# Kernel optimization log

Measured on AMD Instinct MI355X. Metric: run time of the kernel, lower is better.

## Reference

```python
import jax, jax.numpy as jnp
import numpy as np
import math

B, S, D = 4, 2048, 1024
H, DK, DV = 16, 64, 64
EPS = 1e-5
SCALE = math.sqrt(1.0 / D)  # NOTE: original scales by 1/sqrt(d_model), not 1/sqrt(d_k)


def setup_inputs() -> dict:
    key = jax.random.key(0)
    ks = jax.random.split(key, 12)
    s = 0.02
    return {
        "Q": jax.random.normal(ks[0], (B, S, D), jnp.float32),
        "K": jax.random.normal(ks[1], (B, S, D), jnp.float32),
        "V": jax.random.normal(ks[2], (B, S, D), jnp.float32),
        # stacked per-head projection weights (torch Linear: y = x @ W.T + b)
        "Wq": jax.random.normal(ks[3], (H, D, DK), jnp.float32) * s,
        "bq": jnp.zeros((H, DK), jnp.float32),
        "Wk": jax.random.normal(ks[4], (H, D, DK), jnp.float32) * s,
        "bk": jnp.zeros((H, DK), jnp.float32),
        "Wv": jax.random.normal(ks[5], (H, D, DV), jnp.float32) * s,
        "bv": jnp.zeros((H, DV), jnp.float32),
        "Wo": jax.random.normal(ks[6], (H * DV, D), jnp.float32) * s,
        "bo": jnp.zeros((D,), jnp.float32),
        "gamma": jnp.ones((D,), jnp.float32),
        "beta": jnp.zeros((D,), jnp.float32),
    }


def reference(Q, K, V, Wq, bq, Wk, bk, Wv, bv, Wo, bo, gamma, beta):
    residual = Q
    # batched per-head projections: [B,S,D] x [H,D,dk] -> [B,H,S,dk]
    q = jnp.einsum("bsd,hdk->bhsk", Q, Wq) + bq[None, :, None, :]
    k = jnp.einsum("bsd,hdk->bhsk", K, Wk) + bk[None, :, None, :]
    v = jnp.einsum("bsd,hdv->bhsv", V, Wv) + bv[None, :, None, :]
    # scaled dot-product attention (scale uses d_model, per original code)
    attn = jax.nn.softmax(jnp.einsum("bhsk,bhtk->bhst", q, k) * SCALE, axis=-1)
    out = jnp.einsum("bhst,bhtv->bhsv", attn, v)  # [B,H,S,DV]
    # concat heads along feature dim: [B,S,H*DV]
    out = out.transpose(0, 2, 1, 3).reshape(B, S, H * DV)
    out = out @ Wo + bo  # output projection
    # dropout is identity in eval mode
    out = out + residual
    # BatchNorm1d over (B,S) per channel (training-mode batch stats)
    mean = jnp.mean(out, axis=(0, 1))
    var = jnp.mean(jnp.square(out - mean), axis=(0, 1))
    out = (out - mean) * jax.lax.rsqrt(var + EPS) * gamma + beta
    return out.transpose(0, 2, 1)  # (B, d_model, S)
```

## Files before the change

### kernel.cpp

```cpp
#include <hip/hip_runtime.h>

#define B_ 4
#define S_ 2048
#define D_ 1024
#define H_ 16
#define SCALE_ 0.03125f
#define EPS_ 1e-5f
#define NBS_ 8192

typedef unsigned short ushort_t;
typedef __attribute__((ext_vector_type(8))) short short8;
typedef __attribute__((ext_vector_type(4))) short short4v;
typedef __attribute__((ext_vector_type(4))) float floatx4;
typedef __attribute__((ext_vector_type(2))) unsigned int uint2v;

__device__ __forceinline__ ushort_t f2bf(float f) {
  union { float f; unsigned u; } v; v.f = f;
  unsigned r = v.u + 0x7fffu + ((v.u >> 16) & 1u);
  return (ushort_t)(r >> 16);
}

__device__ __forceinline__ float fast_exp2(float x) {
#if __has_builtin(__builtin_amdgcn_exp2f)
  return __builtin_amdgcn_exp2f(x);
#else
  return __expf(x * 0.6931471805599453f);
#endif
}

__device__ __forceinline__ unsigned cvt_pk_bf16(float a, float b) {
  unsigned r;
  asm("v_cvt_pk_bf16_f32 %0, %1, %2" : "=v"(r) : "v"(a), "v"(b));
  return r;
}

__device__ __forceinline__ short8 cvt8(float4 a, float4 b) {
  short8 r;
  r[0] = (short)f2bf(a.x); r[1] = (short)f2bf(a.y);
  r[2] = (short)f2bf(a.z); r[3] = (short)f2bf(a.w);
  r[4] = (short)f2bf(b.x); r[5] = (short)f2bf(b.y);
  r[6] = (short)f2bf(b.z); r[7] = (short)f2bf(b.w);
  return r;
}

__device__ __forceinline__ void gload16(const void* g, void* l) {
  __builtin_amdgcn_global_load_lds(
      (const __attribute__((address_space(1))) unsigned int*)g,
      (__attribute__((address_space(3))) unsigned int*)l, 16, 0, 0);
}

__global__ __launch_bounds__(256) void cvtx_k(const float* __restrict__ src,
                                              ushort_t* __restrict__ dst)
{
  size_t i = ((size_t)blockIdx.x * 256 + threadIdx.x) * 8;
  float4 a = *(const float4*)(src + i);
  float4 b = *(const float4*)(src + i + 4);
  *(short8*)(dst + i) = cvt8(a, b);
}

__global__ __launch_bounds__(256) void wtr_k(const float* __restrict__ src,
                                             ushort_t* __restrict__ dst, int mode)
{
  __shared__ float t[64][65];
  const int tr = blockIdx.x, tc = blockIdx.y;
  const float* sb; int sld;
  if (mode == 0) { sb = src + (size_t)tr * 65536 + (size_t)tc * 64 * 64; sld = 64; }
  else           { sb = src + (size_t)tc * 64 * 1024 + (size_t)tr * 64;  sld = 1024; }
  const int tid = threadIdx.x;
  const int rr = tid >> 2, cs = (tid & 3) * 16;
  const float* p = sb + (size_t)rr * sld + cs;
#pragma unroll
  for (int j = 0; j < 16; ++j) t[rr][cs + j] = p[j];
  __syncthreads();
  ushort_t* dp = dst + (size_t)(tr * 64 + rr) * 1024 + tc * 64 + cs;
#pragma unroll
  for (int j = 0; j < 16; ++j) dp[j] = f2bf(t[cs + j][rr]);
}

__device__ __forceinline__ void xcd_tile(int id, int& m0, int& n0)
{
  m0 = ((id & 7) + 8 * (id >> 6)) * 128;
  n0 = ((id >> 3) & 7) * 128;
}

__device__ __forceinline__ void gemm_mainloop(
    const ushort_t* __restrict__ A, const ushort_t* __restrict__ Bw,
    ushort_t* As, ushort_t* Bs,
    int m0, int n0, int wv, int lane, floatx4 acc[4][2])
{
  const int quad = lane >> 4, l16 = lane & 15;
  const int wm = wv & 1, wn = wv >> 1;
  const int r8 = lane >> 3;
  const int kx = ((lane & 7) ^ r8) * 8;

  auto stage = [&](int buf, int k0) {
#pragma unroll
    for (int j = 0; j < 2; ++j) {
      const int rb = (wv * 2 + j) * 8;
      gload16(A + (size_t)(m0 + rb + r8) * 1024 + k0 + kx,
              (char*)As + buf * 16384 + rb * 128);
      gload16(Bw + (size_t)(n0 + rb + r8) * 1024 + k0 + kx,
              (char*)Bs + buf * 16384 + rb * 128);
    }
  };

  stage(0, 0);
  __syncthreads();

  const int swz = (l16 & 7) << 4;
  for (int it = 0; it < 16; ++it) {
    const int cur = it & 1;
    if (it < 15) stage(cur ^ 1, (it + 1) * 64);
    const char* Ab = (const char*)As + cur * 16384;
    const char* Bb = (const char*)Bs + cur * 16384;
#pragma unroll
    for (int hf = 0; hf < 2; ++hf) {
      short8 af[4], bf[2];
      const int C = (hf * 64 + quad * 16) ^ swz;
#pragma unroll
      for (int i = 0; i < 4; ++i)
        af[i] = *(const short8*)(Ab + (wm * 64 + i * 16 + l16) * 128 + C);
#pragma unroll
      for (int i = 0; i < 2; ++i)
        bf[i] = *(const short8*)(Bb + (wn * 32 + i * 16 + l16) * 128 + C);
#pragma unroll
      for (int mi = 0; mi < 4; ++mi)
#pragma unroll
        for (int ni = 0; ni < 2; ++ni)
          acc[mi][ni] = __builtin_amdgcn_mfma_f32_16x16x32_bf16(
              af[mi], bf[ni], acc[mi][ni], 0, 0, 0);
    }
    __syncthreads();
  }
}

__global__ __launch_bounds__(512) void gemm_proj(
    const ushort_t* __restrict__ A, const ushort_t* __restrict__ Bw,
    const float* __restrict__ bias, ushort_t* __restrict__ outp, float scale)
{
  __shared__ ushort_t As[2 * 128 * 64];
  __shared__ ushort_t Bs[2 * 128 * 64];
  const int tid = threadIdx.x;
  const int wv = tid >> 6, lane = tid & 63, quad = lane >> 4, l16 = lane & 15;
  int m0, n0;
  xcd_tile(blockIdx.x, m0, n0);
  const int wm = wv & 1, wn = wv >> 1;

  floatx4 acc[4][2];
#pragma unroll
  for (int i = 0; i < 4; ++i)
#pragma unroll
    for (int j = 0; j < 2; ++j) acc[i][j] = (floatx4){0.f, 0.f, 0.f, 0.f};

  gemm_mainloop(A, Bw, As, Bs, m0, n0, wv, lane, acc);

  const int b = m0 >> 11;
  const int sbase = (m0 & 2047) + wm * 64;
#pragma unroll
  for (int ni = 0; ni < 2; ++ni) {
    const int c = n0 + wn * 32 + ni * 16 + l16;
    const int h = c >> 6, nn = c & 63;
    const float bs = bias[c];
    ushort_t* op = outp + (size_t)(b * 16 + h) * 2048 * 64 + nn;
#pragma unroll
    for (int mi = 0; mi < 4; ++mi)
#pragma unroll
      for (int r = 0; r < 4; ++r) {
        int s = sbase + mi * 16 + quad * 4 + r;
        op[(size_t)s * 64] = f2bf((acc[mi][ni][r] + bs) * scale);
      }
  }
}

__global__ __launch_bounds__(512) void gemm_projT(
    const ushort_t* __restrict__ A, const ushort_t* __restrict__ Bw,
    const float* __restrict__ bias, ushort_t* __restrict__ outp)
{
  __shared__ ushort_t As[2 * 128 * 64];
  __shared__ ushort_t Bs[2 * 128 * 64];
  const int tid = threadIdx.x;
  const int wv = tid >> 6, lane = tid & 63, quad = lane >> 4, l16 = lane & 15;
  int m0, n0;
  xcd_tile(blockIdx.x, m0, n0);
  const int wm = wv & 1, wn = wv >> 1;

  floatx4 acc[4][2];
#pragma unroll
  for (int i = 0; i < 4; ++i)
#pragma unroll
    for (int j = 0; j < 2; ++j) acc[i][j] = (floatx4){0.f, 0.f, 0.f, 0.f};

  gemm_mainloop(A, Bw, As, Bs, m0, n0, wv, lane, acc);

  const int b = m0 >> 11;
  const int sbase = (m0 & 2047) + wm * 64;
#pragma unroll
  for (int ni = 0; ni < 2; ++ni) {
    const int c = n0 + wn * 32 + ni * 16 + l16;
    const int h = c >> 6, nn = c & 63;
    const float bs = bias[c];
    ushort_t* op = outp + ((size_t)(b * 16 + h) * 64 + nn) * 2048;
#pragma unroll
    for (int mi = 0; mi < 4; ++mi) {
      int s0v = sbase + mi * 16 + quad * 4;
      short4v p;
#pragma unroll
      for (int r = 0; r < 4; ++r) p[r] = (short)f2bf(acc[mi][ni][r] + bs);
      *(short4v*)(op + s0v) = p;
    }
  }
}

__global__ __launch_bounds__(512) void gemm_oproj(
    const ushort_t* __restrict__ A, const ushort_t* __restrict__ Bw,
    const float* __restrict__ bo, const float* __restrict__ resid,
    float* __restrict__ y, float* __restrict__ s1, float* __restrict__ s2)
{
  __shared__ ushort_t As[2 * 128 * 64];
  __shared__ ushort_t Bs[2 * 128 * 64];
  const int tid = threadIdx.x;
  const int wv = tid >> 6, lane = tid & 63, quad = lane >> 4, l16 = lane & 15;
  int m0, n0;
  xcd_tile(blockIdx.x, m0, n0);
  const int wm = wv & 1, wn = wv >> 1;

  floatx4 acc[4][2];
#pragma unroll
  for (int i = 0; i < 4; ++i)
#pragma unroll
    for (int j = 0; j < 2; ++j) acc[i][j] = (floatx4){0.f, 0.f, 0.f, 0.f};

  gemm_mainloop(A, Bw, As, Bs, m0, n0, wv, lane, acc);

  const int mb = m0 + wm * 64;
#pragma unroll
  for (int ni = 0; ni < 2; ++ni) {
    const int d = n0 + wn * 32 + ni * 16 + l16;
    const float bs = bo[d];
    float ps1 = 0.f, ps2 = 0.f;
#pragma unroll
    for (int mi = 0; mi < 4; ++mi)
#pragma unroll
      for (int r = 0; r < 4; ++r) {
        int m = mb + mi * 16 + quad * 4 + r;
        float val = acc[mi][ni][r] + bs + resid[(size_t)m * 1024 + d];
        y[(size_t)m * 1024 + d] = val;
        ps1 += val;
        ps2 += val * val;
      }
    ps1 += __shfl_xor(ps1, 16); ps1 += __shfl_xor(ps1, 32);
    ps2 += __shfl_xor(ps2, 16); ps2 += __shfl_xor(ps2, 32);
    if (quad == 0) {
      atomicAdd(&s1[d], ps1);
      atomicAdd(&s2[d], ps2);
    }
  }
}

__global__ __launch_bounds__(256, 3) void attn_k(
    const ushort_t* __restrict__ q, const ushort_t* __restrict__ k,
    const ushort_t* __restrict__ vt, ushort_t* __restrict__ ao)
{
  __shared__ ushort_t lds[20480];
  char* ldsb = (char*)lds;
  const int tid = threadIdx.x;
  const int wv = tid >> 6, lane = tid & 63, quad = lane >> 4, l16 = lane & 15;

  const int id = blockIdx.x;
  const int j = id >> 3;
  const int pair = (id & 7) + 8 * (j >> 4);
  const int q0 = (j & 15) * 128;
  const int h = pair & 15, b = pair >> 4;

  const size_t bh = (size_t)(b * H_ + h) * S_;
  const ushort_t* vb = vt + (size_t)(b * H_ + h) * 64 * S_;

  short8 aq[2][2];
#pragma unroll
  for (int rb = 0; rb < 2; ++rb) {
    const ushort_t* qrow = q + (bh + q0 + wv * 32 + rb * 16 + l16) * 64;
    aq[rb][0] = *(const short8*)(qrow + quad * 8);
    aq[rb][1] = *(const short8*)(qrow + 32 + quad * 8);
  }

  short8 ones;
#pragma unroll
  for (int j2 = 0; j2 < 8; ++j2) ones[j2] = (short)0x3F80;

  floatx4 o[2][4];
  floatx4 accl[2];
#pragma unroll
  for (int rb = 0; rb < 2; ++rb) {
#pragma unroll
    for (int cb = 0; cb < 4; ++cb) o[rb][cb] = (floatx4){0.f, 0.f, 0.f, 0.f};
    accl[rb] = (floatx4){0.f, 0.f, 0.f, 0.f};
  }

  const int swz = ((l16 & 7) << 4) | (l16 & 8);
  const int q8 = quad * 8;
  const int pb = 32768 + wv * 2048 + l16 * 128;

  auto stage = [&](int nb, int t0) {
#pragma unroll
    for (int i = 0; i < 4; ++i) {
      const int idx = wv * 4 + i;
      const int cb = (idx >> 1) & 3, hf = idx & 1;
      if (idx < 8)
        gload16(k + (bh + t0 + cb * 16 + l16) * 64 + hf * 32 + quad * 8,
                (char*)lds + nb * 8192 + idx * 1024);
      else
        gload16(vb + (size_t)(cb * 16 + l16) * S_ + t0 + hf * 32 + quad * 8,
                (char*)lds + 16384 + nb * 8192 + (idx - 8) * 1024);
    }
  };

  stage(0, 0);
  asm volatile("s_waitcnt vmcnt(0)" ::: "memory");
  __syncthreads();

  for (int t0 = 0; t0 < S_; t0 += 64) {
    const int nb = (t0 >> 6) & 1;
    const ushort_t* KsC = lds + nb * 4096;
    const ushort_t* VsC = lds + 8192 + nb * 4096;
    if (t0 + 64 < S_) stage(nb ^ 1, t0 + 64);

    floatx4 sc[2][4];
#pragma unroll
    for (int rb = 0; rb < 2; ++rb)
#pragma unroll
      for (int cb = 0; cb < 4; ++cb) sc[rb][cb] = (floatx4){0.f, 0.f, 0.f, 0.f};
    __builtin_amdgcn_s_setprio(1);
#pragma unroll
    for (int hf = 0; hf < 2; ++hf) {
      short8 bk[4];
#pragma unroll
      for (int cb = 0; cb < 4; ++cb)
        bk[cb] = *(const short8*)&KsC[(cb * 2 + hf) * 512 + lane * 8];
#pragma unroll
      for (int rb = 0; rb < 2; ++rb)
#pragma unroll
        for (int cb = 0; cb < 4; ++cb)
          sc[rb][cb] = __builtin_amdgcn_mfma_f32_16x16x32_bf16(
              bk[cb], aq[rb][hf], sc[rb][cb], 0, 0, 0);
    }
    __builtin_amdgcn_s_setprio(0);

    short8 bvf[2][4];
#pragma unroll
    for (int hf = 0; hf < 2; ++hf)
#pragma unroll
      for (int cb = 0; cb < 4; ++cb)
        bvf[hf][cb] = *(const short8*)&VsC[(cb * 2 + hf) * 512 + lane * 8];

#pragma unroll
    for (int rb = 0; rb < 2; ++rb) {
#pragma unroll
      for (int cb = 0; cb < 4; ++cb) {
        float p0 = fast_exp2(sc[rb][cb][0]);
        float p1 = fast_exp2(sc[rb][cb][1]);
        float p2 = fast_exp2(sc[rb][cb][2]);
        float p3 = fast_exp2(sc[rb][cb][3]);
        uint2v w;
        w[0] = cvt_pk_bf16(p0, p1);
        w[1] = cvt_pk_bf16(p2, p3);
        *(uint2v*)(ldsb + pb + ((cb * 32 + q8) ^ swz)) = w;
      }
      asm volatile("s_waitcnt lgkmcnt(0)" ::: "memory");
      __builtin_amdgcn_sched_barrier(0);

      __builtin_amdgcn_s_setprio(1);
#pragma unroll
      for (int hf = 0; hf < 2; ++hf) {
        const int lo = (hf * 64 + quad * 16) ^ swz;
        short4v a0 = *(const short4v*)(ldsb + pb + lo);
        short4v a1 = *(const short4v*)(ldsb + pb + (lo ^ 8));
        short8 ap;
        ap[0] = a0[0]; ap[1] = a0[1]; ap[2] = a0[2]; ap[3] = a0[3];
        ap[4] = a1[0]; ap[5] = a1[1]; ap[6] = a1[2]; ap[7] = a1[3];
#pragma unroll
        for (int cb = 0; cb < 4; ++cb)
          o[rb][cb] = __builtin_amdgcn_mfma_f32_16x16x32_bf16(
              ap, bvf[hf][cb], o[rb][cb], 0, 0, 0);
        accl[rb] = __builtin_amdgcn_mfma_f32_16x16x32_bf16(
            ap, ones, accl[rb], 0, 0, 0);
      }
      __builtin_amdgcn_s_setprio(0);
    }

    asm volatile("s_waitcnt vmcnt(0)" ::: "memory");
    __syncthreads();
  }

  float linv[2][4];
#pragma unroll
  for (int rb = 0; rb < 2; ++rb)
#pragma unroll
    for (int r = 0; r < 4; ++r)
      linv[rb][r] = 1.f / accl[rb][r];
#pragma unroll
  for (int rb = 0; rb < 2; ++rb)
#pragma unroll
    for (int cb = 0; cb < 4; ++cb)
#pragma unroll
      for (int r = 0; r < 4; ++r) {
        float val = o[rb][cb][r] * linv[rb][r];
        size_t idx = (size_t)(b * S_ + q0 + wv * 32 + rb * 16 + quad * 4 + r) * 1024
                     + h * 64 + cb * 16 + l16;
        ao[idx] = f2bf(val);
      }
}

__global__ __launch_bounds__(256) void norm_k(
    const float* __restrict__ y, const float* __restrict__ s1,
    const float* __restrict__ s2, const float* __restrict__ gamma,
    const float* __restrict__ beta, float* __restrict__ out)
{
  __shared__ float tile[64][65];
  __shared__ float scl[64], sft[64];
  const int tid = threadIdx.x;
  const int s0 = blockIdx.x * 64, d0 = blockIdx.y * 64, b = blockIdx.z;

  if (tid < 64) {
    int d = d0 + tid;
    float mean = s1[d] * (1.f / (float)NBS_);
    float var = s2[d] * (1.f / (float)NBS_) - mean * mean;
    float rstd = rsqrtf(var + EPS_);
    float g = gamma[d];
    scl[tid] = rstd * g;
    sft[tid] = beta[d] - mean * rstd * g;
  }
  __syncthreads();

  const int si = tid >> 2, dc = (tid & 3) * 16;
  const float* row = y + (size_t)(b * S_ + s0 + si) * D_ + d0 + dc;
#pragma unroll
  for (int j = 0; j < 16; ++j)
    tile[si][dc + j] = row[j] * scl[dc + j] + sft[dc + j];
  __syncthreads();

  const int di = tid >> 2, sg = (tid & 3) * 16;
  float* dst = out + (size_t)(b * D_ + d0 + di) * S_ + s0 + sg;
#pragma unroll
  for (int jj = 0; jj < 4; ++jj) {
    float4 p;
    p.x = tile[sg + jj * 4 + 0][di];
    p.y = tile[sg + jj * 4 + 1][di];
    p.z = tile[sg + jj * 4 + 2][di];
    p.w = tile[sg + jj * 4 + 3][di];
    *(float4*)(dst + jj * 4) = p;
  }
}

extern "C" void kernel_launch(void* const* d_in, const int* in_sizes, int n_in,
                              void* d_out, int out_size, void* d_ws, size_t ws_size,
                              hipStream_t stream)
{
  (void)in_sizes; (void)n_in; (void)out_size; (void)ws_size;
  const float* Q     = (const float*)d_in[0];
  const float* Kin   = (const float*)d_in[1];
  const float* Vin   = (const float*)d_in[2];
  const float* Wq    = (const float*)d_in[3];
  const float* bq    = (const float*)d_in[4];
  const float* Wk    = (const float*)d_in[5];
  const float* bk    = (const float*)d_in[6];
  const float* Wv    = (const float*)d_in[7];
  const float* bv    = (const float*)d_in[8];
  const float* Wo    = (const float*)d_in[9];
  const float* bo    = (const float*)d_in[10];
  const float* gamma = (const float*)d_in[11];
  const float* beta  = (const float*)d_in[12];
  float* out = (float*)d_out;

  char* ws = (char*)d_ws;
  const size_t MB = 1u << 20;
  ushort_t* xb  = (ushort_t*)(ws);
  ushort_t* wtq = (ushort_t*)(ws + 16 * MB);
  ushort_t* wtk = (ushort_t*)(ws + 18 * MB);
  ushort_t* wtv = (ushort_t*)(ws + 20 * MB);
  ushort_t* wto = (ushort_t*)(ws + 22 * MB);
  ushort_t* qb  = (ushort_t*)(ws + 24 * MB);
  ushort_t* kb  = (ushort_t*)(ws + 40 * MB);
  ushort_t* vtb = (ushort_t*)(ws + 56 * MB);
  ushort_t* ao  = (ushort_t*)(ws);
  float*    y   = (float*)(ws + 24 * MB);
  float*    s1  = (float*)(ws + 56 * MB);
  float*    s2  = (float*)(ws + 56 * MB + 4096);

  wtr_k<<<dim3(16, 16), 256, 0, stream>>>(Wq, wtq, 0);
  wtr_k<<<dim3(16, 16), 256, 0, stream>>>(Wk, wtk, 0);
  wtr_k<<<dim3(16, 16), 256, 0, stream>>>(Wv, wtv, 0);
  wtr_k<<<dim3(16, 16), 256, 0, stream>>>(Wo, wto, 1);

  const float QSC = SCALE_ * 1.44269504088896f;
  cvtx_k<<<4096, 256, 0, stream>>>(Q, xb);
  gemm_proj<<<512, 512, 0, stream>>>(xb, wtq, bq, qb, QSC);
  cvtx_k<<<4096, 256, 0, stream>>>(Kin, xb);
  gemm_proj<<<512, 512, 0, stream>>>(xb, wtk, bk, kb, 1.0f);
  cvtx_k<<<4096, 256, 0, stream>>>(Vin, xb);
  gemm_projT<<<512, 512, 0, stream>>>(xb, wtv, bv, vtb);

  attn_k<<<1024, 256, 0, stream>>>(qb, kb, vtb, ao);

  hipMemsetAsync(ws + 56 * MB, 0, 8192, stream);
  gemm_oproj<<<512, 512, 0, stream>>>(ao, wto, bo, Q, y, s1, s2);

  norm_k<<<dim3(32, 16, 4), 256, 0, stream>>>(y, s1, s2, gamma, beta, out);
}
```

Before: 385.3 us.

## Fuse fp32-to-bf16 input conversion into projection GEMM loads and batch weight transposes

```diff
diff --git a/kernel.cpp b/kernel.cpp
--- a/kernel.cpp
+++ b/kernel.cpp
@@ -13,6 +13,7 @@
 typedef __attribute__((ext_vector_type(4))) short short4v;
 typedef __attribute__((ext_vector_type(4))) float floatx4;
 typedef __attribute__((ext_vector_type(2))) unsigned int uint2v;
+typedef __attribute__((ext_vector_type(4))) unsigned int uint4v;
 
 __device__ __forceinline__ ushort_t f2bf(float f) {
   union { float f; unsigned u; } v; v.f = f;
@@ -34,35 +35,26 @@
   return r;
 }
 
-__device__ __forceinline__ short8 cvt8(float4 a, float4 b) {
-  short8 r;
-  r[0] = (short)f2bf(a.x); r[1] = (short)f2bf(a.y);
-  r[2] = (short)f2bf(a.z); r[3] = (short)f2bf(a.w);
-  r[4] = (short)f2bf(b.x); r[5] = (short)f2bf(b.y);
-  r[6] = (short)f2bf(b.z); r[7] = (short)f2bf(b.w);
-  return r;
-}
-
 __device__ __forceinline__ void gload16(const void* g, void* l) {
   __builtin_amdgcn_global_load_lds(
       (const __attribute__((address_space(1))) unsigned int*)g,
       (__attribute__((address_space(3))) unsigned int*)l, 16, 0, 0);
 }
 
-__global__ __launch_bounds__(256) void cvtx_k(const float* __restrict__ src,
-                                              ushort_t* __restrict__ dst)
-{
-  size_t i = ((size_t)blockIdx.x * 256 + threadIdx.x) * 8;
-  float4 a = *(const float4*)(src + i);
-  float4 b = *(const float4*)(src + i + 4);
-  *(short8*)(dst + i) = cvt8(a, b);
-}
-
-__global__ __launch_bounds__(256) void wtr_k(const float* __restrict__ src,
-                                             ushort_t* __restrict__ dst, int mode)
+__global__ __launch_bounds__(256) void wtr_all(
+    const float* __restrict__ Wq, const float* __restrict__ Wk,
+    const float* __restrict__ Wv, const float* __restrict__ Wo,
+    ushort_t* __restrict__ wtq, ushort_t* __restrict__ wtk,
+    ushort_t* __restrict__ wtv, ushort_t* __restrict__ wto)
 {
   __shared__ float t[64][65];
-  const int tr = blockIdx.x, tc = blockIdx.y;
+  const int tr = blockIdx.x, tc = blockIdx.y, z = blockIdx.z;
+  const float* src; ushort_t* dst; int mode;
+  if      (z == 0) { src = Wq; dst = wtq; mode = 0; }
+  else if (z == 1) { src = Wk; dst = wtk; mode = 0; }
+  else if (z == 2) { src = Wv; dst = wtv; mode = 0; }
+  else             { src = Wo; dst = wto; mode = 1; }
+
   const float* sb; int sld;
   if (mode == 0) { sb = src + (size_t)tr * 65536 + (size_t)tc * 64 * 64; sld = 64; }
   else           { sb = src + (size_t)tc * 64 * 1024 + (size_t)tr * 64;  sld = 1024; }
@@ -134,8 +126,84 @@
   }
 }
 
-__global__ __launch_bounds__(512) void gemm_proj(
-    const ushort_t* __restrict__ A, const ushort_t* __restrict__ Bw,
+__device__ __forceinline__ void gemm_mainloop_f32(
+    const float* __restrict__ A, const ushort_t* __restrict__ Bw,
+    ushort_t* As, ushort_t* Bs,
+    int m0, int n0, int wv, int lane, floatx4 acc[4][2])
+{
+  const int quad = lane >> 4, l16 = lane & 15;
+  const int wm = wv & 1, wn = wv >> 1;
+  const int r8 = lane >> 3;
+  const int kx = ((lane & 7) ^ r8) * 8;
+
+  const int row0 = wv * 16 + r8;
+  const int row1 = row0 + 8;
+  const float* a0 = A + (size_t)(m0 + row0) * 1024 + kx;
+  const float* a1 = A + (size_t)(m0 + row1) * 1024 + kx;
+  const int d0 = row0 * 128 + (lane & 7) * 16;
+  const int d1 = row1 * 128 + (lane & 7) * 16;
+
+  float4 av0, av1, av2, av3;
+
+  auto aload = [&](int k0) {
+    av0 = *(const float4*)(a0 + k0);
+    av1 = *(const float4*)(a0 + k0 + 4);
+    av2 = *(const float4*)(a1 + k0);
+    av3 = *(const float4*)(a1 + k0 + 4);
+  };
+  auto awrite = [&](int buf) {
+    uint4v w0, w1;
+    w0[0] = cvt_pk_bf16(av0.x, av0.y); w0[1] = cvt_pk_bf16(av0.z, av0.w);
+    w0[2] = cvt_pk_bf16(av1.x, av1.y); w0[3] = cvt_pk_bf16(av1.z, av1.w);
+    w1[0] = cvt_pk_bf16(av2.x, av2.y); w1[1] = cvt_pk_bf16(av2.z, av2.w);
+    w1[2] = cvt_pk_bf16(av3.x, av3.y); w1[3] = cvt_pk_bf16(av3.z, av3.w);
+    *(uint4v*)((char*)As + buf * 16384 + d0) = w0;
+    *(uint4v*)((char*)As + buf * 16384 + d1) = w1;
+  };
+  auto stageB = [&](int buf, int k0) {
+#pragma unroll
+    for (int j = 0; j < 2; ++j) {
+      const int rb = (wv * 2 + j) * 8;
+      gload16(Bw + (size_t)(n0 + rb + r8) * 1024 + k0 + kx,
+              (char*)Bs + buf * 16384 + rb * 128);
+    }
+  };
+
+  aload(0);
+  stageB(0, 0);
+  awrite(0);
+  __syncthreads();
+
+  const int swz = (l16 & 7) << 4;
+  for (int it = 0; it < 16; ++it) {
+    const int cur = it & 1;
+    if (it < 15) { aload((it + 1) * 64); stageB(cur ^ 1, (it + 1) * 64); }
+    const char* Ab = (const char*)As + cur * 16384;
+    const char* Bb = (const char*)Bs + cur * 16384;
+#pragma unroll
+    for (int hf = 0; hf < 2; ++hf) {
+      short8 af[4], bf[2];
+      const int C = (hf * 64 + quad * 16) ^ swz;
+#pragma unroll
+      for (int i = 0; i < 4; ++i)
+        af[i] = *(const short8*)(Ab + (wm * 64 + i * 16 + l16) * 128 + C);
+#pragma unroll
+      for (int i = 0; i < 2; ++i)
+        bf[i] = *(const short8*)(Bb + (wn * 32 + i * 16 + l16) * 128 + C);
+#pragma unroll
+      for (int mi = 0; mi < 4; ++mi)
+#pragma unroll
+        for (int ni = 0; ni < 2; ++ni)
+          acc[mi][ni] = __builtin_amdgcn_mfma_f32_16x16x32_bf16(
+              af[mi], bf[ni], acc[mi][ni], 0, 0, 0);
+    }
+    if (it < 15) awrite(cur ^ 1);
+    __syncthreads();
+  }
+}
+
+__global__ __launch_bounds__(512) void gemm_projF(
+    const float* __restrict__ A, const ushort_t* __restrict__ Bw,
     const float* __restrict__ bias, ushort_t* __restrict__ outp, float scale)
 {
   __shared__ ushort_t As[2 * 128 * 64];
@@ -152,7 +220,7 @@
 #pragma unroll
     for (int j = 0; j < 2; ++j) acc[i][j] = (floatx4){0.f, 0.f, 0.f, 0.f};
 
-  gemm_mainloop(A, Bw, As, Bs, m0, n0, wv, lane, acc);
+  gemm_mainloop_f32(A, Bw, As, Bs, m0, n0, wv, lane, acc);
 
   const int b = m0 >> 11;
   const int sbase = (m0 & 2047) + wm * 64;
@@ -172,8 +240,8 @@
   }
 }
 
-__global__ __launch_bounds__(512) void gemm_projT(
-    const ushort_t* __restrict__ A, const ushort_t* __restrict__ Bw,
+__global__ __launch_bounds__(512) void gemm_projTF(
+    const float* __restrict__ A, const ushort_t* __restrict__ Bw,
     const float* __restrict__ bias, ushort_t* __restrict__ outp)
 {
   __shared__ ushort_t As[2 * 128 * 64];
@@ -190,7 +258,7 @@
 #pragma unroll
     for (int j = 0; j < 2; ++j) acc[i][j] = (floatx4){0.f, 0.f, 0.f, 0.f};
 
-  gemm_mainloop(A, Bw, As, Bs, m0, n0, wv, lane, acc);
+  gemm_mainloop_f32(A, Bw, As, Bs, m0, n0, wv, lane, acc);
 
   const int b = m0 >> 11;
   const int sbase = (m0 & 2047) + wm * 64;
@@ -473,7 +541,6 @@
 
   char* ws = (char*)d_ws;
   const size_t MB = 1u << 20;
-  ushort_t* xb  = (ushort_t*)(ws);
   ushort_t* wtq = (ushort_t*)(ws + 16 * MB);
   ushort_t* wtk = (ushort_t*)(ws + 18 * MB);
   ushort_t* wtv = (ushort_t*)(ws + 20 * MB);
@@ -486,18 +553,13 @@
   float*    s1  = (float*)(ws + 56 * MB);
   float*    s2  = (float*)(ws + 56 * MB + 4096);
 
-  wtr_k<<<dim3(16, 16), 256, 0, stream>>>(Wq, wtq, 0);
-  wtr_k<<<dim3(16, 16), 256, 0, stream>>>(Wk, wtk, 0);
-  wtr_k<<<dim3(16, 16), 256, 0, stream>>>(Wv, wtv, 0);
-  wtr_k<<<dim3(16, 16), 256, 0, stream>>>(Wo, wto, 1);
+  wtr_all<<<dim3(16, 16, 4), 256, 0, stream>>>(Wq, Wk, Wv, Wo,
+                                               wtq, wtk, wtv, wto);
 
   const float QSC = SCALE_ * 1.44269504088896f;
-  cvtx_k<<<4096, 256, 0, stream>>>(Q, xb);
-  gemm_proj<<<512, 512, 0, stream>>>(xb, wtq, bq, qb, QSC);
-  cvtx_k<<<4096, 256, 0, stream>>>(Kin, xb);
-  gemm_proj<<<512, 512, 0, stream>>>(xb, wtk, bk, kb, 1.0f);
-  cvtx_k<<<4096, 256, 0, stream>>>(Vin, xb);
-  gemm_projT<<<512, 512, 0, stream>>>(xb, wtv, bv, vtb);
+  gemm_projF <<<512, 512, 0, stream>>>(Q,   wtq, bq, qb, QSC);
+  gemm_projF <<<512, 512, 0, stream>>>(Kin, wtk, bk, kb, 1.0f);
+  gemm_projTF<<<512, 512, 0, stream>>>(Vin, wtv, bv, vtb);
 
   attn_k<<<1024, 256, 0, stream>>>(qb, kb, vtb, ao);
 
```

New measurement: 390.1 us. About the same (+1.2%).
